# Kernel optimization log

Measured on AMD Instinct MI355X. Metric: run time of the kernel, lower is better.

Reference implementation:

```python
import jax, jax.numpy as jnp
import numpy as np

W_RAD = 2  # box-filter radius (init kwarg w)
KSIZE = 2 * W_RAD + 1


def _box_conv3d(x, kernel):
    # x: [B,1,D,H,W], kernel: [1,1,k,k,k]; 'same' padding, stride 1
    return jax.lax.conv_general_dilated(
        x, kernel,
        window_strides=(1, 1, 1),
        padding=[(W_RAD, W_RAD)] * 3,
        dimension_numbers=("NCDHW", "OIDHW", "NCDHW"),
    )


def setup_inputs() -> dict:
    key = jax.random.key(0)
    k1, k2 = jax.random.split(key)
    shape = (2, 1, 160, 160, 160)
    M = jax.random.uniform(k1, shape, dtype=jnp.float32)
    R = jax.random.uniform(k2, shape, dtype=jnp.float32)
    kernel = jnp.ones((1, 1, KSIZE, KSIZE, KSIZE), dtype=jnp.float32) / (KSIZE ** 3)
    return {"M": M, "R": R, "kernel": kernel}


def reference(M, R, kernel):
    M_m = _box_conv3d(M, kernel)
    R_m = _box_conv3d(R, kernel)
    MM_m = _box_conv3d(M * M, kernel)
    RR_m = _box_conv3d(R * R, kernel)
    MR_m = _box_conv3d(M * R, kernel)
    M_var = jnp.sqrt(MM_m - M_m ** 2 + 1e-05)
    R_var = jnp.sqrt(RR_m - R_m ** 2 + 1e-05)
    corr = (MR_m - M_m * R_m) / (M_var * R_var + 1e-05)
    return -jnp.mean(corr)
```

## Files before the change

### kernel.cpp

```cpp
#include <hip/hip_runtime.h>
#include <math.h>

#define Bsz 2
#define Dd 160
#define Hh 160
#define Ww 160
#define TH 8
#define TW 32
#define DCHUNK 40
#define NCH 5

__global__ void lncc_zero(float* out) { out[0] = 0.0f; }

__global__ __launch_bounds__(256)
void lncc_main(const float* __restrict__ M,
               const float* __restrict__ R,
               const float* __restrict__ kern,
               float* __restrict__ out)
{
    __shared__ float lm[TH + 4][TW + 5];
    __shared__ float lr[TH + 4][TW + 5];
    __shared__ float sw[NCH][TH + 4][TW + 1];
    __shared__ float red[4];

    const int tid = threadIdx.x;
    const int tx  = tid & 31;
    const int ty  = tid >> 5;

    const int w0 = blockIdx.x * TW;
    const int h0 = blockIdx.y * TH;
    const int b  = blockIdx.z >> 2;
    const int d0 = (blockIdx.z & 3) * DCHUNK;

    const float k0 = kern[0];

    float ring[5][NCH];
#pragma unroll
    for (int t = 0; t < 5; ++t)
#pragma unroll
        for (int c = 0; c < NCH; ++c) ring[t][c] = 0.0f;

    float acc = 0.0f;

    for (int s = 0; s < DCHUNK + 4; ++s) {
        const int  dd  = d0 - 2 + s;
        const bool dok = (dd >= 0) && (dd < Dd);
        const size_t slice = (size_t)(b * Dd + (dok ? dd : 0)) * Hh * Ww;
        const float* Mp = M + slice;
        const float* Rp = R + slice;

        for (int i = tid; i < (TH + 4) * (TW + 4); i += 256) {
            int yy = i / (TW + 4);
            int xx = i - yy * (TW + 4);
            int gh = h0 + yy - 2;
            int gw = w0 + xx - 2;
            float vm = 0.0f, vr = 0.0f;
            if (dok && gh >= 0 && gh < Hh && gw >= 0 && gw < Ww) {
                size_t o = (size_t)gh * Ww + gw;
                vm = Mp[o];
                vr = Rp[o];
            }
            lm[yy][xx] = vm;
            lr[yy][xx] = vr;
        }
        __syncthreads();

        for (int i = tid; i < (TH + 4) * TW; i += 256) {
            int yy = i >> 5;
            int x  = i & 31;
            float sm = 0.f, sr = 0.f, smm = 0.f, srr = 0.f, smr = 0.f;
#pragma unroll
            for (int t = 0; t < 5; ++t) {
                float a  = lm[yy][x + t];
                float bb = lr[yy][x + t];
                sm += a;
                sr += bb;
                smm = fmaf(a, a, smm);
                srr = fmaf(bb, bb, srr);
                smr = fmaf(a, bb, smr);
            }
            sw[0][yy][x] = sm;
            sw[1][yy][x] = sr;
            sw[2][yy][x] = smm;
            sw[3][yy][x] = srr;
            sw[4][yy][x] = smr;
        }
        __syncthreads();

        float pl[NCH];
#pragma unroll
        for (int c = 0; c < NCH; ++c) {
            float v = 0.0f;
#pragma unroll
            for (int j = 0; j < 5; ++j) v += sw[c][ty + j][tx];
            pl[c] = v;
        }

#pragma unroll
        for (int t = 0; t < 4; ++t)
#pragma unroll
            for (int c = 0; c < NCH; ++c) ring[t][c] = ring[t + 1][c];
#pragma unroll
        for (int c = 0; c < NCH; ++c) ring[4][c] = pl[c];

        if (s >= 4) {
            float S[NCH];
#pragma unroll
            for (int c = 0; c < NCH; ++c)
                S[c] = ring[0][c] + ring[1][c] + ring[2][c] + ring[3][c] + ring[4][c];
            float Mm  = S[0] * k0;
            float Rm  = S[1] * k0;
            float MMm = S[2] * k0;
            float RRm = S[3] * k0;
            float MRm = S[4] * k0;
            float Mv = sqrtf(MMm - Mm * Mm + 1e-5f);
            float Rv = sqrtf(RRm - Rm * Rm + 1e-5f);
            acc += (MRm - Mm * Rm) / (Mv * Rv + 1e-5f);
        }
    }

#pragma unroll
    for (int off = 32; off > 0; off >>= 1)
        acc += __shfl_down(acc, off, 64);
    if ((tid & 63) == 0) red[tid >> 6] = acc;
    __syncthreads();
    if (tid == 0) {
        float t = red[0] + red[1] + red[2] + red[3];
        atomicAdd(out, -t * (1.0f / 8192000.0f));
    }
}

extern "C" void kernel_launch(void* const* d_in, const int* in_sizes, int n_in,
                              void* d_out, int out_size, void* d_ws, size_t ws_size,
                              hipStream_t stream) {
    const float* M = (const float*)d_in[0];
    const float* R = (const float*)d_in[1];
    const float* K = (const float*)d_in[2];
    float* out = (float*)d_out;

    lncc_zero<<<1, 1, 0, stream>>>(out);

    dim3 grid(Ww / TW, Hh / TH, Bsz * (Dd / DCHUNK));
    lncc_main<<<grid, 256, 0, stream>>>(M, R, K, out);
}
```

Baseline: 163.7 us.

## Prefetch next depth slice into registers and retile blocks for 512 threads

```diff
diff --git a/kernel.cpp b/kernel.cpp
--- a/kernel.cpp
+++ b/kernel.cpp
@@ -5,23 +5,29 @@
 #define Dd 160
 #define Hh 160
 #define Ww 160
-#define TH 8
+#define TH 16
 #define TW 32
-#define DCHUNK 40
+#define DCHUNK 20
 #define NCH 5
+#define NT 512
+#define HALO_H (TH + 4)
+#define HALO_W (TW + 4)
+#define APIX (HALO_H * HALO_W)
+#define BPIX (HALO_H * TW)
+#define NSLICE (DCHUNK + 5)
 
 __global__ void lncc_zero(float* out) { out[0] = 0.0f; }
 
-__global__ __launch_bounds__(256)
+__global__ __launch_bounds__(NT)
 void lncc_main(const float* __restrict__ M,
                const float* __restrict__ R,
                const float* __restrict__ kern,
                float* __restrict__ out)
 {
-    __shared__ float lm[TH + 4][TW + 5];
-    __shared__ float lr[TH + 4][TW + 5];
-    __shared__ float sw[NCH][TH + 4][TW + 1];
-    __shared__ float red[4];
+    __shared__ float lm[HALO_H][HALO_W + 1];
+    __shared__ float lr[HALO_H][HALO_W + 1];
+    __shared__ float sw[NCH][HALO_H][TW + 1];
+    __shared__ float red[NT / 64];
 
     const int tid = threadIdx.x;
     const int tx  = tid & 31;
@@ -29,10 +35,44 @@
 
     const int w0 = blockIdx.x * TW;
     const int h0 = blockIdx.y * TH;
-    const int b  = blockIdx.z >> 2;
-    const int d0 = (blockIdx.z & 3) * DCHUNK;
+    const int b  = blockIdx.z >> 3;
+    const int d0 = (blockIdx.z & 7) * DCHUNK;
 
     const float k0 = kern[0];
+
+    int  g_off[2], l_off[2];
+    bool g_ok[2], l_act[2];
+#pragma unroll
+    for (int p = 0; p < 2; ++p) {
+        int i = tid + p * NT;
+        bool act = (i < APIX);
+        int yy = act ? (i / HALO_W) : 0;
+        int xx = act ? (i - yy * HALO_W) : 0;
+        int gh = h0 + yy - 2;
+        int gw = w0 + xx - 2;
+        l_act[p] = act;
+        g_ok[p]  = act && gh >= 0 && gh < Hh && gw >= 0 && gw < Ww;
+        g_off[p] = gh * Ww + gw;
+        l_off[p] = yy * (HALO_W + 1) + xx;
+    }
+    float* lmf = &lm[0][0];
+    float* lrf = &lr[0][0];
+
+    const size_t batch_base = (size_t)b * Dd * Hh * Ww;
+
+    float pm[2], pr[2];
+    auto issue = [&](int s) {
+        int  dd  = d0 - 2 + s;
+        bool dok = (dd >= 0) && (dd < Dd);
+        const float* Mp = M + batch_base + (size_t)(dok ? dd : 0) * (Hh * Ww);
+        const float* Rp = R + batch_base + (size_t)(dok ? dd : 0) * (Hh * Ww);
+#pragma unroll
+        for (int p = 0; p < 2; ++p) {
+            bool ok = dok && g_ok[p];
+            pm[p] = ok ? Mp[g_off[p]] : 0.0f;
+            pr[p] = ok ? Rp[g_off[p]] : 0.0f;
+        }
+    };
 
     float ring[5][NCH];
 #pragma unroll
@@ -42,80 +82,70 @@
 
     float acc = 0.0f;
 
-    for (int s = 0; s < DCHUNK + 4; ++s) {
-        const int  dd  = d0 - 2 + s;
-        const bool dok = (dd >= 0) && (dd < Dd);
-        const size_t slice = (size_t)(b * Dd + (dok ? dd : 0)) * Hh * Ww;
-        const float* Mp = M + slice;
-        const float* Rp = R + slice;
+    issue(0);
 
-        for (int i = tid; i < (TH + 4) * (TW + 4); i += 256) {
-            int yy = i / (TW + 4);
-            int xx = i - yy * (TW + 4);
-            int gh = h0 + yy - 2;
-            int gw = w0 + xx - 2;
-            float vm = 0.0f, vr = 0.0f;
-            if (dok && gh >= 0 && gh < Hh && gw >= 0 && gw < Ww) {
-                size_t o = (size_t)gh * Ww + gw;
-                vm = Mp[o];
-                vr = Rp[o];
-            }
-            lm[yy][xx] = vm;
-            lr[yy][xx] = vr;
-        }
-        __syncthreads();
-
-        for (int i = tid; i < (TH + 4) * TW; i += 256) {
-            int yy = i >> 5;
-            int x  = i & 31;
-            float sm = 0.f, sr = 0.f, smm = 0.f, srr = 0.f, smr = 0.f;
+    for (int s5 = 0; s5 < NSLICE; s5 += 5) {
 #pragma unroll
-            for (int t = 0; t < 5; ++t) {
-                float a  = lm[yy][x + t];
-                float bb = lr[yy][x + t];
-                sm += a;
-                sr += bb;
-                smm = fmaf(a, a, smm);
-                srr = fmaf(bb, bb, srr);
-                smr = fmaf(a, bb, smr);
-            }
-            sw[0][yy][x] = sm;
-            sw[1][yy][x] = sr;
-            sw[2][yy][x] = smm;
-            sw[3][yy][x] = srr;
-            sw[4][yy][x] = smr;
-        }
-        __syncthreads();
-
-        float pl[NCH];
-#pragma unroll
-        for (int c = 0; c < NCH; ++c) {
-            float v = 0.0f;
-#pragma unroll
-            for (int j = 0; j < 5; ++j) v += sw[c][ty + j][tx];
-            pl[c] = v;
-        }
+        for (int so = 0; so < 5; ++so) {
+            const int s = s5 + so;
 
 #pragma unroll
-        for (int t = 0; t < 4; ++t)
+            for (int p = 0; p < 2; ++p) {
+                if (l_act[p]) {
+                    lmf[l_off[p]] = pm[p];
+                    lrf[l_off[p]] = pr[p];
+                }
+            }
+            __syncthreads();
+
+            if (s + 1 < NSLICE) issue(s + 1);
+
 #pragma unroll
-            for (int c = 0; c < NCH; ++c) ring[t][c] = ring[t + 1][c];
+            for (int p = 0; p < 2; ++p) {
+                int i = tid + p * NT;
+                if (i < BPIX) {
+                    int yy = i >> 5;
+                    int x  = i & 31;
+                    float sm = 0.f, sr = 0.f, smm = 0.f, srr = 0.f, smr = 0.f;
 #pragma unroll
-        for (int c = 0; c < NCH; ++c) ring[4][c] = pl[c];
+                    for (int t = 0; t < 5; ++t) {
+                        float a  = lm[yy][x + t];
+                        float bb = lr[yy][x + t];
+                        sm += a;
+                        sr += bb;
+                        smm = fmaf(a, a, smm);
+                        srr = fmaf(bb, bb, srr);
+                        smr = fmaf(a, bb, smr);
+                    }
+                    sw[0][yy][x] = sm;
+                    sw[1][yy][x] = sr;
+                    sw[2][yy][x] = smm;
+                    sw[3][yy][x] = srr;
+                    sw[4][yy][x] = smr;
+                }
+            }
+            __syncthreads();
 
-        if (s >= 4) {
-            float S[NCH];
 #pragma unroll
-            for (int c = 0; c < NCH; ++c)
-                S[c] = ring[0][c] + ring[1][c] + ring[2][c] + ring[3][c] + ring[4][c];
-            float Mm  = S[0] * k0;
-            float Rm  = S[1] * k0;
-            float MMm = S[2] * k0;
-            float RRm = S[3] * k0;
-            float MRm = S[4] * k0;
-            float Mv = sqrtf(MMm - Mm * Mm + 1e-5f);
-            float Rv = sqrtf(RRm - Rm * Rm + 1e-5f);
-            acc += (MRm - Mm * Rm) / (Mv * Rv + 1e-5f);
+            for (int c = 0; c < NCH; ++c) {
+                ring[so][c] = sw[c][ty][tx] + sw[c][ty + 1][tx] + sw[c][ty + 2][tx]
+                            + sw[c][ty + 3][tx] + sw[c][ty + 4][tx];
+            }
+
+            if (s >= 4 && s < DCHUNK + 4) {
+                float S[NCH];
+#pragma unroll
+                for (int c = 0; c < NCH; ++c)
+                    S[c] = ring[0][c] + ring[1][c] + ring[2][c] + ring[3][c] + ring[4][c];
+                float Mm  = S[0] * k0;
+                float Rm  = S[1] * k0;
+                float MMm = S[2] * k0;
+                float RRm = S[3] * k0;
+                float MRm = S[4] * k0;
+                float Mv = sqrtf(MMm - Mm * Mm + 1e-5f);
+                float Rv = sqrtf(RRm - Rm * Rm + 1e-5f);
+                acc += (MRm - Mm * Rm) / (Mv * Rv + 1e-5f);
+            }
         }
     }
 
@@ -125,7 +155,9 @@
     if ((tid & 63) == 0) red[tid >> 6] = acc;
     __syncthreads();
     if (tid == 0) {
-        float t = red[0] + red[1] + red[2] + red[3];
+        float t = 0.f;
+#pragma unroll
+        for (int i = 0; i < NT / 64; ++i) t += red[i];
         atomicAdd(out, -t * (1.0f / 8192000.0f));
     }
 }
@@ -141,5 +173,5 @@
     lncc_zero<<<1, 1, 0, stream>>>(out);
 
     dim3 grid(Ww / TW, Hh / TH, Bsz * (Dd / DCHUNK));
-    lncc_main<<<grid, 256, 0, stream>>>(M, R, K, out);
+    lncc_main<<<grid, NT, 0, stream>>>(M, R, K, out);
 }
```

New measurement: 143.2 us. -12.5%, faster.
